# Performance work log

Measured on AMD Instinct MI355X. Metric: run time of the kernel, lower is better.

Reference implementation:

```python
import jax, jax.numpy as jnp
import numpy as np

VOCAB = 50000; T = 4096; EMBED = 500; H = 500  # hidden per direction (HIDDEN_SIZE=1000, bidirectional)
NUM_TAGS = 16; START = 14; STOP = 15
NEG = -10000.0


def setup_inputs() -> dict:
    key = jax.random.key(0)
    ks = jax.random.split(key, 16)
    n = lambda k, s, sc=0.1: (jax.random.normal(k, s) * sc).astype(jnp.float32)
    trans = n(ks[12], (NUM_TAGS, NUM_TAGS), 1.0)
    trans = trans.at[START, :].set(NEG).at[:, STOP].set(NEG)  # as in __init__
    return {
        "sent": jax.random.randint(ks[0], (T,), 0, VOCAB),
        "embed_w": n(ks[1], (VOCAB, EMBED), 1.0),
        "wih0": n(ks[2], (2, 4 * H, EMBED)),
        "whh0": n(ks[3], (2, 4 * H, H)),
        "bih0": n(ks[4], (2, 4 * H)),
        "bhh0": n(ks[5], (2, 4 * H)),
        "wih1": n(ks[6], (2, 4 * H, 2 * H)),
        "whh1": n(ks[7], (2, 4 * H, H)),
        "bih1": n(ks[8], (2, 4 * H)),
        "bhh1": n(ks[9], (2, 4 * H)),
        "w_out": n(ks[10], (NUM_TAGS, 2 * H)),
        "b_out": n(ks[11], (NUM_TAGS,)),
        "trans": trans,
        "h0": n(ks[13], (4, H), 1.0),  # init_hidden() uses randn; layout [layer*2+dir, H]
        "c0": n(ks[14], (4, H), 1.0),
    }


def _lstm_dir(x, wih, whh, bih, bhh, h0, c0):
    b = bih + bhh
    def cell(carry, xt):
        h, c = carry
        g = xt @ wih.T + h @ whh.T + b          # [4H], torch gate order i,f,g,o
        i, f, gg, o = jnp.split(g, 4)
        c = jax.nn.sigmoid(f) * c + jax.nn.sigmoid(i) * jnp.tanh(gg)
        h = jax.nn.sigmoid(o) * jnp.tanh(c)
        return (h, c), h
    _, hs = jax.lax.scan(cell, (h0, c0), x)
    return hs  # [T, H]


def _bilstm_layer(x, wih, whh, bih, bhh, h0, c0):
    fwd = _lstm_dir(x, wih[0], whh[0], bih[0], bhh[0], h0[0], c0[0])
    bwd = _lstm_dir(x[::-1], wih[1], whh[1], bih[1], bhh[1], h0[1], c0[1])[::-1]
    return jnp.concatenate([fwd, bwd], axis=-1)  # [T, 2H]


def _features(sent, embed_w, wih0, whh0, bih0, bhh0, wih1, whh1, bih1, bhh1, w_out, b_out, h0, c0):
    x = embed_w[sent]                                            # [T, EMBED]
    x = _bilstm_layer(x, wih0, whh0, bih0, bhh0, h0[0:2], c0[0:2])
    x = _bilstm_layer(x, wih1, whh1, bih1, bhh1, h0[2:4], c0[2:4])
    return x @ w_out.T + b_out                                   # [T, NUM_TAGS]


def _viterbi(feats, trans):
    score0 = jnp.full((NUM_TAGS,), NEG, dtype=feats.dtype).at[START].set(0.0)
    def step(score, feat):
        m = score[None, :] + trans               # m[tag, prev] = score[prev] + trans[tag, prev]
        return jnp.max(m, axis=1) + feat, jnp.argmax(m, axis=1)
    score, bptr = jax.lax.scan(step, score0, feats)              # bptr: [T, NUM_TAGS]
    score = score + trans[STOP]
    best_tag = jnp.argmax(score)
    best_score = score[best_tag]
    # faithful to the source backtrace: best_tag is NOT updated inside its loop,
    # so path = [bptr[1][bt], ..., bptr[T-1][bt], bt]
    path = jnp.concatenate([bptr[1:, best_tag], best_tag[None]])
    return best_score, path


def reference(sent, embed_w, wih0, whh0, bih0, bhh0, wih1, whh1, bih1, bhh1, w_out, b_out, trans, h0, c0):
    feats = _features(sent, embed_w, wih0, whh0, bih0, bhh0,
                      wih1, whh1, bih1, bhh1, w_out, b_out, h0, c0)
    return _viterbi(feats, trans)
```

## Files before the change

### kernel.cpp

```cpp
#include <hip/hip_runtime.h>


#define T_SEQ 4096
#define HPAD  512
#define NTAG  16


__global__ void embed_k(const int* __restrict__ sent, const float* __restrict__ ew,
                        float* __restrict__ x0) {
  int t = blockIdx.x;
  int row = sent[t];
  for (int k = threadIdx.x; k < HPAD; k += blockDim.x)
    x0[(size_t)t * HPAD + k] = (k < 500) ? ew[(size_t)row * 500 + k] : 0.0f;
}

__global__ __launch_bounds__(256) void gin_gemm_k(
    const float* __restrict__ A, int KA,
    const float* __restrict__ wih, const float* __restrict__ bih,
    const float* __restrict__ bhh, int Kreal, float* __restrict__ G) {
  const int dir = blockIdx.z;
  const int bm = blockIdx.y, bn = blockIdx.x;
  const float* W = wih + (size_t)dir * 2000 * Kreal;

  __shared__ float As[16][128];
  __shared__ float Bs[16][128];

  const int tid = threadIdx.x;
  const int tx = tid & 15, ty = tid >> 4;
  float acc[8][8] = {};

  for (int k0 = 0; k0 < KA; k0 += 16) {
#pragma unroll
    for (int q = 0; q < 2; q++) {
      int f4 = tid + q * 256;
      int m = f4 >> 2, kc = (f4 & 3) * 4;
      float4 av = *reinterpret_cast<const float4*>(A + (size_t)(bm * 128 + m) * KA + k0 + kc);
      As[kc + 0][m] = av.x; As[kc + 1][m] = av.y;
      As[kc + 2][m] = av.z; As[kc + 3][m] = av.w;
    }
#pragma unroll
    for (int q = 0; q < 2; q++) {
      int f4 = tid + q * 256;
      int n = f4 >> 2, kc = (f4 & 3) * 4;
      int nn = bn * 128 + n;
      int gate = nn >> 9, j = nn & 511;
      int k = k0 + kc;
      int jk = k & 511, half = k >> 9;
      float4 bv = {0.0f, 0.0f, 0.0f, 0.0f};
      if (j < 500 && jk < 500)
        bv = *reinterpret_cast<const float4*>(
            &W[(size_t)(gate * 500 + j) * Kreal + half * 500 + jk]);
      Bs[kc + 0][n] = bv.x; Bs[kc + 1][n] = bv.y;
      Bs[kc + 2][n] = bv.z; Bs[kc + 3][n] = bv.w;
    }
    __syncthreads();
#pragma unroll
    for (int kk = 0; kk < 16; kk++) {
      float a[8], b[8];
      *reinterpret_cast<float4*>(&a[0]) = *reinterpret_cast<const float4*>(&As[kk][ty * 8]);
      *reinterpret_cast<float4*>(&a[4]) = *reinterpret_cast<const float4*>(&As[kk][ty * 8 + 4]);
      *reinterpret_cast<float4*>(&b[0]) = *reinterpret_cast<const float4*>(&Bs[kk][tx * 8]);
      *reinterpret_cast<float4*>(&b[4]) = *reinterpret_cast<const float4*>(&Bs[kk][tx * 8 + 4]);
#pragma unroll
      for (int i = 0; i < 8; i++)
#pragma unroll
        for (int j = 0; j < 8; j++) acc[i][j] = fmaf(a[i], b[j], acc[i][j]);
    }
    __syncthreads();
  }
#pragma unroll
  for (int i = 0; i < 8; i++) {
#pragma unroll
    for (int j = 0; j < 8; j++) {
      int m = bm * 128 + ty * 8 + i;
      int nn = bn * 128 + tx * 8 + j;
      int gate = nn >> 9, ju = nn & 511;
      float o = 0.0f;
      if (ju < 500) {
        int r = gate * 500 + ju;
        o = acc[i][j] + bih[dir * 2000 + r] + bhh[dir * 2000 + r];
      }
      G[((size_t)dir * T_SEQ + m) * 2048 + nn] = o;
    }
  }
}

__device__ __forceinline__ unsigned long long pack_hv(unsigned tag, float h) {
  return (unsigned long long)tag | ((unsigned long long)__float_as_uint(h) << 32);
}

__device__ __forceinline__ float fsig(float x) {
  float e = __expf(-x);
  return __builtin_amdgcn_rcpf(1.0f + e);
}
__device__ __forceinline__ float ftanhf(float x) {
  return fmaf(2.0f, fsig(x + x), -1.0f);
}

__global__ void hinit_k(const float* __restrict__ h0, int layer,
                        unsigned long long* __restrict__ hcomm) {
  int i = blockIdx.x * blockDim.x + threadIdx.x;
  int dir = i >> 10, par = (i >> 9) & 1, j = i & 511;
  unsigned long long v;
  if (par == 0) {
    float h = (j < 500) ? h0[(layer * 2 + dir) * 500 + j] : 0.0f;
    v = pack_hv(0u, h);
  } else {
    v = 0xFFFFFFFFull;
  }
  hcomm[(size_t)(dir * 2 + par) * HPAD + j] = v;
}

__global__ __launch_bounds__(1024)
__attribute__((amdgpu_waves_per_eu(4, 4)))
void lstm_k(
    const float* __restrict__ whh_base,
    const float* __restrict__ gin,
    const float* __restrict__ c0,
    float* __restrict__ xout,
    unsigned long long* __restrict__ hcomm,
    int layer) {
  __shared__ float part[16][68];
  __shared__ float hbuf[16][32];

  const int tid = threadIdx.x;
  const int dir = blockIdx.x >> 5;
  const int wgd = blockIdx.x & 31;
  const int w = tid >> 6;
  const int lane = tid & 63;

  const int gate = lane >> 4;
  const int ul   = lane & 15;
  const int j    = wgd * 16 + ul;
  const int row  = gate * 500 + j;

  float wreg[32];
  const float* Wd = whh_base + (size_t)dir * 2000 * 500;
#pragma unroll
  for (int i = 0; i < 32; i++) {
    int k = w * 32 + i;
    wreg[i] = (j < 500 && k < 500) ? Wd[(size_t)row * 500 + k] : 0.0f;
  }
#pragma unroll
  for (int i = 0; i < 32; i++) asm volatile("" : "+v"(wreg[i]));

  float c = 0.0f;
  if (w == 0 && lane < 16 && j < 500) c = c0[(layer * 2 + dir) * 500 + j];

  unsigned long long* hcd = hcomm + (size_t)dir * 2 * HPAD;
  bool dead = false;

  for (int t = 0; t < T_SEQ; t++) {
    const int t_in = (dir == 0) ? t : (T_SEQ - 1 - t);

    float gi = 0.0f;
    if (w == 0) {
      const float* gb = gin + ((size_t)dir * T_SEQ + t_in) * 2048;
      gi = gb[gate * 512 + j];
    }

    unsigned long long v = 0;
    if (!dead) {
      const unsigned long long* hp =
          hcd + (size_t)(t & 1) * HPAD + w * 32 + (lane & 31);
      int guard = 0;
      for (;;) {
        v = __hip_atomic_load(hp, __ATOMIC_RELAXED, __HIP_MEMORY_SCOPE_AGENT);
        if (__all((int)((unsigned)v == (unsigned)t))) break;
        if (++guard > (1 << 22)) { dead = true; break; }
      }
    }
    float hval = __uint_as_float((unsigned)(v >> 32));

    if (lane < 32) hbuf[w][lane] = hval;
    float a = 0.0f;
#pragma unroll
    for (int b = 0; b < 8; b++) {
      float4 hv = *reinterpret_cast<const float4*>(&hbuf[w][b * 4]);
      a = fmaf(wreg[b * 4 + 0], hv.x, a);
      a = fmaf(wreg[b * 4 + 1], hv.y, a);
      a = fmaf(wreg[b * 4 + 2], hv.z, a);
      a = fmaf(wreg[b * 4 + 3], hv.w, a);
    }
    part[w][lane] = a;
    __syncthreads();

    if (w == 0) {
      __builtin_amdgcn_s_setprio(1);
      float p0 = part[0][lane] + part[1][lane];
      float p1 = part[2][lane] + part[3][lane];
      float p2 = part[4][lane] + part[5][lane];
      float p3 = part[6][lane] + part[7][lane];
      float p4 = part[8][lane] + part[9][lane];
      float p5 = part[10][lane] + part[11][lane];
      float p6 = part[12][lane] + part[13][lane];
      float p7 = part[14][lane] + part[15][lane];
      float q0 = p0 + p1, q1 = p2 + p3, q2 = p4 + p5, q3 = p6 + p7;
      float s = gi + ((q0 + q1) + (q2 + q3));
      float nl = (gate == 2) ? ftanhf(s) : fsig(s);
      float xf = __shfl(nl, lane + 16, 64);
      float xg = __shfl(nl, lane + 32, 64);
      float xo = __shfl(nl, lane + 48, 64);
      if (lane < 16) {
        c = xf * c + nl * xg;
        float h = xo * ftanhf(c);
        __hip_atomic_store(hcd + (size_t)((t + 1) & 1) * HPAD + j,
                           pack_hv((unsigned)(t + 1), h),
                           __ATOMIC_RELAXED, __HIP_MEMORY_SCOPE_AGENT);
        if (j < 500)
          xout[(size_t)t_in * 1024 + (size_t)dir * HPAD + j] = h;
      }
      __builtin_amdgcn_s_setprio(0);
    }
  }
}

__global__ __launch_bounds__(256) void feats_k(
    const float* __restrict__ x2, const float* __restrict__ w_out,
    const float* __restrict__ b_out, float* __restrict__ feats) {
  int tid = threadIdx.x;
  int tag = tid & 15, tl = tid >> 4;
  int t = blockIdx.x * 16 + tl;
  float a0 = 0.0f, a1 = 0.0f, a2 = 0.0f, a3 = 0.0f;
  for (int k = 0; k < 1024; k += 4) {
    int jk = k & 511;
    const float* xr = x2 + (size_t)t * 1024 + k;
    const float* wr = w_out + tag * 1000 + (k >> 9) * 500 + jk;
    if (jk + 3 < 500) {
      a0 = fmaf(xr[0], wr[0], a0);
      a1 = fmaf(xr[1], wr[1], a1);
      a2 = fmaf(xr[2], wr[2], a2);
      a3 = fmaf(xr[3], wr[3], a3);
    } else if (jk < 500) {
#pragma unroll
      for (int e = 0; e < 4; e++)
        if (jk + e < 500) a0 = fmaf(xr[e], wr[e], a0);
    }
  }
  feats[t * 16 + tag] = ((a0 + a1) + (a2 + a3)) + b_out[tag];
}

__global__ __launch_bounds__(64) void viterbi_k(
    const float* __restrict__ feats, const float* __restrict__ trans,
    int* __restrict__ bptr, float* __restrict__ out) {
  int tid = threadIdx.x;
  int tag = tid & 15, pg = tid >> 4;
  float tr0 = trans[tag * 16 + pg * 4 + 0];
  float tr1 = trans[tag * 16 + pg * 4 + 1];
  float tr2 = trans[tag * 16 + pg * 4 + 2];
  float tr3 = trans[tag * 16 + pg * 4 + 3];
  float s = (tag == 14) ? 0.0f : -10000.0f;
  float ft = feats[tag];
  for (int t = 0; t < T_SEQ; t++) {
    float ftn = (t + 1 < T_SEQ) ? feats[(t + 1) * 16 + tag] : 0.0f;
    float c0 = __shfl(s, pg * 4 + 0, 64) + tr0;
    float c1 = __shfl(s, pg * 4 + 1, 64) + tr1;
    float c2 = __shfl(s, pg * 4 + 2, 64) + tr2;
    float c3 = __shfl(s, pg * 4 + 3, 64) + tr3;
    float bv = c0; int bi = pg * 4;
    if (c1 > bv) { bv = c1; bi = pg * 4 + 1; }
    if (c2 > bv) { bv = c2; bi = pg * 4 + 2; }
    if (c3 > bv) { bv = c3; bi = pg * 4 + 3; }
    float ov = __shfl_xor(bv, 16, 64); int oi = __shfl_xor(bi, 16, 64);
    if (ov > bv || (ov == bv && oi < bi)) { bv = ov; bi = oi; }
    ov = __shfl_xor(bv, 32, 64); oi = __shfl_xor(bi, 32, 64);
    if (ov > bv || (ov == bv && oi < bi)) { bv = ov; bi = oi; }
    s = bv + ft;
    ft = ftn;
    if (pg == 0) bptr[t * 16 + tag] = bi;
  }
  s += trans[15 * 16 + tag];
  float bv = s; int bi = tag;
  for (int mask = 1; mask < 16; mask <<= 1) {
    float ov = __shfl_xor(bv, mask, 16); int oi = __shfl_xor(bi, mask, 16);
    if (ov > bv || (ov == bv && oi < bi)) { bv = ov; bi = oi; }
  }
  if (tid == 0) out[0] = bv;
  int bt = bi;
  for (int i = tid; i < T_SEQ - 1; i += 64)
    out[1 + i] = (float)bptr[(i + 1) * 16 + bt];
  if (tid == 0) out[T_SEQ] = (float)bt;
}

extern "C" void kernel_launch(void* const* d_in, const int* in_sizes, int n_in,
                              void* d_out, int out_size, void* d_ws, size_t ws_size,
                              hipStream_t stream) {
  const int*   sent  = (const int*)d_in[0];
  const float* embed = (const float*)d_in[1];
  const float* wih0  = (const float*)d_in[2];
  const float* whh0  = (const float*)d_in[3];
  const float* bih0  = (const float*)d_in[4];
  const float* bhh0  = (const float*)d_in[5];
  const float* wih1  = (const float*)d_in[6];
  const float* whh1  = (const float*)d_in[7];
  const float* bih1  = (const float*)d_in[8];
  const float* bhh1  = (const float*)d_in[9];
  const float* w_out = (const float*)d_in[10];
  const float* b_out = (const float*)d_in[11];
  const float* trans = (const float*)d_in[12];
  const float* h0    = (const float*)d_in[13];
  const float* c0    = (const float*)d_in[14];
  float* out = (float*)d_out;

  char* ws = (char*)d_ws;
  float* x0    = (float*)(ws + 0);
  float* x1    = (float*)(ws + 8388608);
  float* x2    = (float*)(ws + 25165824);
  float* gin   = (float*)(ws + 41943040);
  float* feats = (float*)(ws + 109051904);
  int*   bptr  = (int*)(ws + 109314048);
  unsigned long long* hcomm = (unsigned long long*)(ws + 109576192);

  embed_k<<<T_SEQ, 256, 0, stream>>>(sent, embed, x0);

  gin_gemm_k<<<dim3(16, 32, 2), 256, 0, stream>>>(x0, 512, wih0, bih0, bhh0, 500, gin);
  hinit_k<<<2, 1024, 0, stream>>>(h0, 0, hcomm);
  lstm_k<<<64, 1024, 0, stream>>>(whh0, gin, c0, x1, hcomm, 0);

  gin_gemm_k<<<dim3(16, 32, 2), 256, 0, stream>>>(x1, 1024, wih1, bih1, bhh1, 1000, gin);
  hinit_k<<<2, 1024, 0, stream>>>(h0, 1, hcomm);
  lstm_k<<<64, 1024, 0, stream>>>(whh1, gin, c0, x2, hcomm, 1);

  feats_k<<<T_SEQ / 16, 256, 0, stream>>>(x2, w_out, b_out, feats);
  viterbi_k<<<1, 64, 0, stream>>>(feats, trans, bptr, out);
}
```

Baseline: 13.11 ms.

## Fuse embedding gather into input GEMM and double-buffer its shared tiles

The separate embedding kernel is removed. The first input-projection GEMM now gathers embedding rows directly through a per-block token index cached in shared memory. The GEMM also switches to double-buffered shared-memory tiles, loading the next K-slice into registers while the current one is consumed, which removes one sync per iteration. The gains are one fewer launch, no padded intermediate write/read, and overlap of global loads with FMA work, paid for with twice the LDS footprint and more live registers. The whole runtime is likely dominated by the sequential LSTM kernels, so the effect on total time should be small.

Measured after the change: 13.16 ms. No clear change (+0.4%).

```diff
diff --git a/kernel.cpp b/kernel.cpp
--- a/kernel.cpp
+++ b/kernel.cpp
@@ -6,68 +6,98 @@
 #define NTAG  16
 
 
-__global__ void embed_k(const int* __restrict__ sent, const float* __restrict__ ew,
-                        float* __restrict__ x0) {
-  int t = blockIdx.x;
-  int row = sent[t];
-  for (int k = threadIdx.x; k < HPAD; k += blockDim.x)
-    x0[(size_t)t * HPAD + k] = (k < 500) ? ew[(size_t)row * 500 + k] : 0.0f;
-}
-
 __global__ __launch_bounds__(256) void gin_gemm_k(
     const float* __restrict__ A, int KA,
+    const int* __restrict__ sent, const float* __restrict__ embed_w,
     const float* __restrict__ wih, const float* __restrict__ bih,
     const float* __restrict__ bhh, int Kreal, float* __restrict__ G) {
   const int dir = blockIdx.z;
   const int bm = blockIdx.y, bn = blockIdx.x;
   const float* W = wih + (size_t)dir * 2000 * Kreal;
 
-  __shared__ float As[16][128];
-  __shared__ float Bs[16][128];
+  __shared__ float As[2][16][128];
+  __shared__ float Bs[2][16][128];
+  __shared__ int   sSent[128];
 
   const int tid = threadIdx.x;
   const int tx = tid & 15, ty = tid >> 4;
+
+  if (sent && tid < 128) sSent[tid] = sent[bm * 128 + tid];
+  if (sent) __syncthreads();
+
+  const int mA[2] = { (tid + 0) >> 2, (tid + 256) >> 2 };
+  const int kA[2] = { ((tid + 0) & 3) * 4, ((tid + 256) & 3) * 4 };
+
+  auto loadA = [&](int k0, int q) -> float4 {
+    int m = mA[q], kc = kA[q];
+    int k = k0 + kc;
+    if (sent) {
+      float4 z = {0.f, 0.f, 0.f, 0.f};
+      if (k < 500)
+        z = *reinterpret_cast<const float4*>(&embed_w[(size_t)sSent[m] * 500 + k]);
+      return z;
+    }
+    return *reinterpret_cast<const float4*>(&A[(size_t)(bm * 128 + m) * KA + k]);
+  };
+  auto loadB = [&](int k0, int q) -> float4 {
+    int n = mA[q], kc = kA[q];
+    int nn = bn * 128 + n;
+    int gate = nn >> 9, j = nn & 511;
+    int k = k0 + kc;
+    int jk = k & 511, half = k >> 9;
+    float4 z = {0.f, 0.f, 0.f, 0.f};
+    if (j < 500 && jk < 500)
+      z = *reinterpret_cast<const float4*>(
+          &W[(size_t)(gate * 500 + j) * Kreal + half * 500 + jk]);
+    return z;
+  };
+  auto store = [&](int buf, int q, float4 av, float4 bv) {
+    int m = mA[q], kc = kA[q];
+    As[buf][kc + 0][m] = av.x; As[buf][kc + 1][m] = av.y;
+    As[buf][kc + 2][m] = av.z; As[buf][kc + 3][m] = av.w;
+    Bs[buf][kc + 0][m] = bv.x; Bs[buf][kc + 1][m] = bv.y;
+    Bs[buf][kc + 2][m] = bv.z; Bs[buf][kc + 3][m] = bv.w;
+  };
+
+  {
+    float4 a0 = loadA(0, 0), b0 = loadB(0, 0);
+    float4 a1 = loadA(0, 1), b1 = loadB(0, 1);
+    store(0, 0, a0, b0);
+    store(0, 1, a1, b1);
+  }
+  __syncthreads();
+
+  const int iters = KA >> 4;
   float acc[8][8] = {};
 
-  for (int k0 = 0; k0 < KA; k0 += 16) {
-#pragma unroll
-    for (int q = 0; q < 2; q++) {
-      int f4 = tid + q * 256;
-      int m = f4 >> 2, kc = (f4 & 3) * 4;
-      float4 av = *reinterpret_cast<const float4*>(A + (size_t)(bm * 128 + m) * KA + k0 + kc);
-      As[kc + 0][m] = av.x; As[kc + 1][m] = av.y;
-      As[kc + 2][m] = av.z; As[kc + 3][m] = av.w;
-    }
-#pragma unroll
-    for (int q = 0; q < 2; q++) {
-      int f4 = tid + q * 256;
-      int n = f4 >> 2, kc = (f4 & 3) * 4;
-      int nn = bn * 128 + n;
-      int gate = nn >> 9, j = nn & 511;
-      int k = k0 + kc;
-      int jk = k & 511, half = k >> 9;
-      float4 bv = {0.0f, 0.0f, 0.0f, 0.0f};
-      if (j < 500 && jk < 500)
-        bv = *reinterpret_cast<const float4*>(
-            &W[(size_t)(gate * 500 + j) * Kreal + half * 500 + jk]);
-      Bs[kc + 0][n] = bv.x; Bs[kc + 1][n] = bv.y;
-      Bs[kc + 2][n] = bv.z; Bs[kc + 3][n] = bv.w;
-    }
-    __syncthreads();
+  for (int it = 0; it < iters; ++it) {
+    const int cur = it & 1;
+    const bool hasNext = (it + 1 < iters);
+    float4 aP0, bP0, aP1, bP1;
+    if (hasNext) {
+      int k0n = (it + 1) << 4;
+      aP0 = loadA(k0n, 0); bP0 = loadB(k0n, 0);
+      aP1 = loadA(k0n, 1); bP1 = loadB(k0n, 1);
+    }
 #pragma unroll
     for (int kk = 0; kk < 16; kk++) {
       float a[8], b[8];
-      *reinterpret_cast<float4*>(&a[0]) = *reinterpret_cast<const float4*>(&As[kk][ty * 8]);
-      *reinterpret_cast<float4*>(&a[4]) = *reinterpret_cast<const float4*>(&As[kk][ty * 8 + 4]);
-      *reinterpret_cast<float4*>(&b[0]) = *reinterpret_cast<const float4*>(&Bs[kk][tx * 8]);
-      *reinterpret_cast<float4*>(&b[4]) = *reinterpret_cast<const float4*>(&Bs[kk][tx * 8 + 4]);
+      *reinterpret_cast<float4*>(&a[0]) = *reinterpret_cast<const float4*>(&As[cur][kk][ty * 8]);
+      *reinterpret_cast<float4*>(&a[4]) = *reinterpret_cast<const float4*>(&As[cur][kk][ty * 8 + 4]);
+      *reinterpret_cast<float4*>(&b[0]) = *reinterpret_cast<const float4*>(&Bs[cur][kk][tx * 8]);
+      *reinterpret_cast<float4*>(&b[4]) = *reinterpret_cast<const float4*>(&Bs[cur][kk][tx * 8 + 4]);
 #pragma unroll
       for (int i = 0; i < 8; i++)
 #pragma unroll
         for (int j = 0; j < 8; j++) acc[i][j] = fmaf(a[i], b[j], acc[i][j]);
     }
+    if (hasNext) {
+      store(cur ^ 1, 0, aP0, bP0);
+      store(cur ^ 1, 1, aP1, bP1);
+    }
     __syncthreads();
   }
+
 #pragma unroll
   for (int i = 0; i < 8; i++) {
 #pragma unroll
@@ -303,7 +333,6 @@
   float* out = (float*)d_out;
 
   char* ws = (char*)d_ws;
-  float* x0    = (float*)(ws + 0);
   float* x1    = (float*)(ws + 8388608);
   float* x2    = (float*)(ws + 25165824);
   float* gin   = (float*)(ws + 41943040);
@@ -311,13 +340,13 @@
   int*   bptr  = (int*)(ws + 109314048);
   unsigned long long* hcomm = (unsigned long long*)(ws + 109576192);
 
-  embed_k<<<T_SEQ, 256, 0, stream>>>(sent, embed, x0);
-
-  gin_gemm_k<<<dim3(16, 32, 2), 256, 0, stream>>>(x0, 512, wih0, bih0, bhh0, 500, gin);
+  gin_gemm_k<<<dim3(16, 32, 2), 256, 0, stream>>>(nullptr, 512, sent, embed,
+                                                  wih0, bih0, bhh0, 500, gin);
   hinit_k<<<2, 1024, 0, stream>>>(h0, 0, hcomm);
   lstm_k<<<64, 1024, 0, stream>>>(whh0, gin, c0, x1, hcomm, 0);
 
-  gin_gemm_k<<<dim3(16, 32, 2), 256, 0, stream>>>(x1, 1024, wih1, bih1, bhh1, 1000, gin);
+  gin_gemm_k<<<dim3(16, 32, 2), 256, 0, stream>>>(x1, 1024, nullptr, nullptr,
+                                                  wih1, bih1, bhh1, 1000, gin);
   hinit_k<<<2, 1024, 0, stream>>>(h0, 1, hcomm);
   lstm_k<<<64, 1024, 0, stream>>>(whh1, gin, c0, x2, hcomm, 1);
 
```
